# Kernel optimization log

Measured on AMD Instinct MI355X. Metric: run time of the kernel, lower is better.

Reference implementation:

```python
import jax, jax.numpy as jnp
import numpy as np

B, N, FIELD_DIM, OUT_DIM = 65536, 128, 16, 64


def setup_inputs() -> dict:
    key = jax.random.key(0)
    k1, k2 = jax.random.split(key)
    x = jax.random.normal(k1, (B, N), dtype=jnp.float32)
    # learned FFM kernel: (n_features, field_dim, output_dim), uniform init like keras 'uniform'
    kernel = jax.random.uniform(k2, (N, FIELD_DIM, OUT_DIM), dtype=jnp.float32, minval=-0.05, maxval=0.05)
    # feature i belongs to field i % FIELD_DIM (the field_dict of the layer)
    field_dict = jnp.arange(N, dtype=jnp.int32) % FIELD_DIM
    return {"x": x, "kernel": kernel, "field_dict": field_dict}


def reference(x, kernel, field_dict):
    # Original math: out_b = sum_{i<j} <kernel[i, fd[j]], kernel[j, fd[i]]> * x[b,i] * x[b,j]
    n = kernel.shape[0]
    # A[i, j, k] = kernel[i, field_dict[j], k]  -> [N, N, OUT_DIM] (small: 128*128*64)
    A = kernel[:, field_dict, :]
    # S[i, j] = <kernel[i, fd[j]], kernel[j, fd[i]]>
    S = jnp.einsum('ijk,jik->ij', A, A)
    mask = jnp.triu(jnp.ones((n, n), dtype=S.dtype), k=1)  # i < j only
    Sm = S * mask
    # bilinear form per sample: sum_{i<j} S_ij x_i x_j
    return jnp.einsum('bi,ij,bj->b', x, Sm, x)
```

## Files before the change

kernel.cpp:

```cpp
#include <hip/hip_runtime.h>

#define NB 65536
#define NN 128
#define FDIM 16
#define ODIM 64

typedef __attribute__((ext_vector_type(8))) short s16x8;
typedef __attribute__((ext_vector_type(4))) float f32x4;
typedef __attribute__((address_space(3))) void lds_void_t;
typedef const __attribute__((address_space(1))) void gbl_void_t;

__device__ __forceinline__ unsigned short f2bf_rne(float f) {
    unsigned u = __builtin_bit_cast(unsigned, f);
    u += 0x7FFFu + ((u >> 16) & 1u);
    return (unsigned short)(u >> 16);
}
__device__ __forceinline__ float bf2f(unsigned short h) {
    unsigned u = ((unsigned)h) << 16;
    return __builtin_bit_cast(float, u);
}

__device__ __forceinline__ int xswz(int m, int c) {
    int g = (c >> 3) ^ ((m >> 2) << 1);
    return m * 128 + g * 8 + (c & 7);
}

__global__ __launch_bounds__(256) void prep_w_fast(const float* __restrict__ kern,
                                                   const int* __restrict__ fd,
                                                   unsigned short* __restrict__ wfrag) {
    int d = blockIdx.x * 32 + (threadIdx.x >> 3);
    int i = d >> 7, j = d & 127;
    int part = threadIdx.x & 7;
    int fi = fd[i], fj = fd[j];
    const float4* ap = (const float4*)(kern + (i * FDIM + fj) * ODIM + part * 8);
    const float4* bp = (const float4*)(kern + (j * FDIM + fi) * ODIM + part * 8);
    float4 a0 = ap[0], a1 = ap[1];
    float4 b0 = bp[0], b1 = bp[1];
    float s = a0.x * b0.x + a0.y * b0.y + a0.z * b0.z + a0.w * b0.w +
              a1.x * b1.x + a1.y * b1.y + a1.z * b1.z + a1.w * b1.w;
    s += __shfl_xor(s, 1, 64);
    s += __shfl_xor(s, 2, 64);
    s += __shfl_xor(s, 4, 64);
    if (part == 0) {
        float w = (i == j) ? 0.f : 0.5f * s;
        int kt = i >> 5, kc = (i >> 3) & 3, e = i & 7;
        wfrag[(((j >> 4) * 4 + kt) * 64 + kc * 16 + (j & 15)) * 8 + e] = f2bf_rne(w);
    }
}

__global__ __launch_bounds__(256, 2) void qform(const float* __restrict__ x,
                                                const unsigned short* __restrict__ wfrag,
                                                float* __restrict__ out) {
    __shared__ __align__(16) unsigned short wlds[16384];
    __shared__ __align__(16) unsigned short xlds[8][2048];

    const int tid = threadIdx.x;
    const int bid = blockIdx.x;

    {
        const char* gsrc = (const char*)wfrag;
        char* ldst = (char*)wlds;
#pragma unroll
        for (int t = 0; t < 8; ++t) {
            int off = t * 4096 + tid * 16;
            __builtin_amdgcn_global_load_lds((gbl_void_t*)(gsrc + off),
                                             (lds_void_t*)(ldst + off), 16, 0, 0);
        }
    }

    const int wave = tid >> 6, lane = tid & 63;
    const int row = lane & 15, kc = lane >> 4;
    const int t0 = wave * 2, t1 = t0 + 1;
    const size_t base = (size_t)bid * 128;
    const float* xp0 = x + (base + (size_t)(t0 * 16 + row)) * NN;
    const float* xp1 = x + (base + (size_t)(t1 * 16 + row)) * NN;

    s16x8 ah0[4], al0[4], ah1[4], al1[4];
#pragma unroll
    for (int kt = 0; kt < 4; ++kt) {
        const float4* p0 = (const float4*)(xp0 + kt * 32 + kc * 8);
        const float4* p1 = (const float4*)(xp1 + kt * 32 + kc * 8);
        float4 v00 = p0[0], v01 = p0[1], v10 = p1[0], v11 = p1[1];
        float vs0[8] = {v00.x, v00.y, v00.z, v00.w, v01.x, v01.y, v01.z, v01.w};
        float vs1[8] = {v10.x, v10.y, v10.z, v10.w, v11.x, v11.y, v11.z, v11.w};
        s16x8 hv0, hv1;
#pragma unroll
        for (int e = 0; e < 8; ++e) {
            unsigned short h0 = f2bf_rne(vs0[e]);
            unsigned short h1 = f2bf_rne(vs1[e]);
            hv0[e] = (short)h0; hv1[e] = (short)h1;
            ah0[kt][e] = (short)h0; ah1[kt][e] = (short)h1;
            float l0f = vs0[e] - bf2f(h0);
            float l1f = vs1[e] - bf2f(h1);
            al0[kt][e] = (short)(unsigned short)(__builtin_bit_cast(unsigned, l0f) >> 16);
            al1[kt][e] = (short)(unsigned short)(__builtin_bit_cast(unsigned, l1f) >> 16);
        }
        *(s16x8*)&xlds[t0][xswz(row, kt * 32 + kc * 8)] = hv0;
        *(s16x8*)&xlds[t1][xswz(row, kt * 32 + kc * 8)] = hv1;
    }
    __syncthreads();

    f32x4 acc0[8], acc1[8];
#pragma unroll
    for (int nt = 0; nt < 8; ++nt) {
        f32x4 c0 = {0.f, 0.f, 0.f, 0.f}, c1 = {0.f, 0.f, 0.f, 0.f};
#pragma unroll
        for (int kt = 0; kt < 4; ++kt) {
            s16x8 bf = *(const s16x8*)&wlds[((nt * 4 + kt) * 64 + lane) * 8];
            c0 = __builtin_amdgcn_mfma_f32_16x16x32_bf16(ah0[kt], bf, c0, 0, 0, 0);
            c0 = __builtin_amdgcn_mfma_f32_16x16x32_bf16(al0[kt], bf, c0, 0, 0, 0);
            c1 = __builtin_amdgcn_mfma_f32_16x16x32_bf16(ah1[kt], bf, c1, 0, 0, 0);
            c1 = __builtin_amdgcn_mfma_f32_16x16x32_bf16(al1[kt], bf, c1, 0, 0, 0);
        }
        acc0[nt] = c0; acc1[nt] = c1;
    }

    const int rg = lane >> 4, cl = lane & 15;
    float q00 = 0, q01 = 0, q02 = 0, q03 = 0;
    float q10 = 0, q11 = 0, q12 = 0, q13 = 0;
#pragma unroll
    for (int nt = 0; nt < 8; ++nt) {
        int c = nt * 16 + cl;
        q00 += acc0[nt][0] * bf2f(xlds[t0][xswz(rg * 4 + 0, c)]);
        q01 += acc0[nt][1] * bf2f(xlds[t0][xswz(rg * 4 + 1, c)]);
        q02 += acc0[nt][2] * bf2f(xlds[t0][xswz(rg * 4 + 2, c)]);
        q03 += acc0[nt][3] * bf2f(xlds[t0][xswz(rg * 4 + 3, c)]);
        q10 += acc1[nt][0] * bf2f(xlds[t1][xswz(rg * 4 + 0, c)]);
        q11 += acc1[nt][1] * bf2f(xlds[t1][xswz(rg * 4 + 1, c)]);
        q12 += acc1[nt][2] * bf2f(xlds[t1][xswz(rg * 4 + 2, c)]);
        q13 += acc1[nt][3] * bf2f(xlds[t1][xswz(rg * 4 + 3, c)]);
    }
#pragma unroll
    for (int m = 1; m <= 8; m <<= 1) {
        q00 += __shfl_xor(q00, m, 64); q01 += __shfl_xor(q01, m, 64);
        q02 += __shfl_xor(q02, m, 64); q03 += __shfl_xor(q03, m, 64);
        q10 += __shfl_xor(q10, m, 64); q11 += __shfl_xor(q11, m, 64);
        q12 += __shfl_xor(q12, m, 64); q13 += __shfl_xor(q13, m, 64);
    }
    if (cl == 0) {
        float* o0 = out + base + t0 * 16 + rg * 4;
        float* o1 = out + base + t1 * 16 + rg * 4;
        o0[0] = q00; o0[1] = q01; o0[2] = q02; o0[3] = q03;
        o1[0] = q10; o1[1] = q11; o1[2] = q12; o1[3] = q13;
    }
}

extern "C" void kernel_launch(void* const* d_in, const int* in_sizes, int n_in,
                              void* d_out, int out_size, void* d_ws, size_t ws_size,
                              hipStream_t stream) {
    const float* x = (const float*)d_in[0];
    const float* kern = (const float*)d_in[1];
    const int* fd = (const int*)d_in[2];
    float* out = (float*)d_out;
    unsigned short* wfrag = (unsigned short*)d_ws;

    prep_w_fast<<<dim3(512), dim3(256), 0, stream>>>(kern, fd, wfrag);
    qform<<<dim3(512), dim3(256), 0, stream>>>(x, wfrag, out);
}
```

Before: 18.71 us.

## Drop bf16 low-part split MFMAs and re-read fp32 x from global for epilogue

Removes the hi/lo bf16 split of x, so each tile needs half as many MFMAs and fewer registers. The x LDS staging buffer is gone. The epilogue now reads fp32 x straight from global/L2 and fuses the dot products into the MFMA loop instead of holding all accumulators. Occupancy hint rises to 4 blocks and the output store is vectorised. The cost is accuracy: x enters the MFMA only as single bf16, while the epilogue multiplier is now full fp32.

```diff
diff --git a/kernel.cpp b/kernel.cpp
--- a/kernel.cpp
+++ b/kernel.cpp
@@ -14,15 +14,6 @@
     unsigned u = __builtin_bit_cast(unsigned, f);
     u += 0x7FFFu + ((u >> 16) & 1u);
     return (unsigned short)(u >> 16);
-}
-__device__ __forceinline__ float bf2f(unsigned short h) {
-    unsigned u = ((unsigned)h) << 16;
-    return __builtin_bit_cast(float, u);
-}
-
-__device__ __forceinline__ int xswz(int m, int c) {
-    int g = (c >> 3) ^ ((m >> 2) << 1);
-    return m * 128 + g * 8 + (c & 7);
 }
 
 __global__ __launch_bounds__(256) void prep_w_fast(const float* __restrict__ kern,
@@ -48,11 +39,10 @@
     }
 }
 
-__global__ __launch_bounds__(256, 2) void qform(const float* __restrict__ x,
+__global__ __launch_bounds__(256, 4) void qform(const float* __restrict__ x,
                                                 const unsigned short* __restrict__ wfrag,
                                                 float* __restrict__ out) {
     __shared__ __align__(16) unsigned short wlds[16384];
-    __shared__ __align__(16) unsigned short xlds[8][2048];
 
     const int tid = threadIdx.x;
     const int bid = blockIdx.x;
@@ -72,35 +62,31 @@
     const int row = lane & 15, kc = lane >> 4;
     const int t0 = wave * 2, t1 = t0 + 1;
     const size_t base = (size_t)bid * 128;
-    const float* xp0 = x + (base + (size_t)(t0 * 16 + row)) * NN;
-    const float* xp1 = x + (base + (size_t)(t1 * 16 + row)) * NN;
+    const float* xp0 = x + (base + (size_t)(t0 * 16 + row)) * NN + kc * 8;
+    const float* xp1 = x + (base + (size_t)(t1 * 16 + row)) * NN + kc * 8;
 
-    s16x8 ah0[4], al0[4], ah1[4], al1[4];
+    s16x8 ah0[4], ah1[4];
 #pragma unroll
     for (int kt = 0; kt < 4; ++kt) {
-        const float4* p0 = (const float4*)(xp0 + kt * 32 + kc * 8);
-        const float4* p1 = (const float4*)(xp1 + kt * 32 + kc * 8);
+        const float4* p0 = (const float4*)(xp0 + kt * 32);
+        const float4* p1 = (const float4*)(xp1 + kt * 32);
         float4 v00 = p0[0], v01 = p0[1], v10 = p1[0], v11 = p1[1];
         float vs0[8] = {v00.x, v00.y, v00.z, v00.w, v01.x, v01.y, v01.z, v01.w};
         float vs1[8] = {v10.x, v10.y, v10.z, v10.w, v11.x, v11.y, v11.z, v11.w};
-        s16x8 hv0, hv1;
 #pragma unroll
         for (int e = 0; e < 8; ++e) {
-            unsigned short h0 = f2bf_rne(vs0[e]);
-            unsigned short h1 = f2bf_rne(vs1[e]);
-            hv0[e] = (short)h0; hv1[e] = (short)h1;
-            ah0[kt][e] = (short)h0; ah1[kt][e] = (short)h1;
-            float l0f = vs0[e] - bf2f(h0);
-            float l1f = vs1[e] - bf2f(h1);
-            al0[kt][e] = (short)(unsigned short)(__builtin_bit_cast(unsigned, l0f) >> 16);
-            al1[kt][e] = (short)(unsigned short)(__builtin_bit_cast(unsigned, l1f) >> 16);
+            ah0[kt][e] = (short)f2bf_rne(vs0[e]);
+            ah1[kt][e] = (short)f2bf_rne(vs1[e]);
         }
-        *(s16x8*)&xlds[t0][xswz(row, kt * 32 + kc * 8)] = hv0;
-        *(s16x8*)&xlds[t1][xswz(row, kt * 32 + kc * 8)] = hv1;
     }
     __syncthreads();
 
-    f32x4 acc0[8], acc1[8];
+    const int rg = lane >> 4, cl = lane & 15;
+    const float* e0 = x + (base + (size_t)(t0 * 16 + rg * 4)) * NN + cl;
+    const float* e1 = x + (base + (size_t)(t1 * 16 + rg * 4)) * NN + cl;
+
+    float q00 = 0, q01 = 0, q02 = 0, q03 = 0;
+    float q10 = 0, q11 = 0, q12 = 0, q13 = 0;
 #pragma unroll
     for (int nt = 0; nt < 8; ++nt) {
         f32x4 c0 = {0.f, 0.f, 0.f, 0.f}, c1 = {0.f, 0.f, 0.f, 0.f};
@@ -108,27 +94,17 @@
         for (int kt = 0; kt < 4; ++kt) {
             s16x8 bf = *(const s16x8*)&wlds[((nt * 4 + kt) * 64 + lane) * 8];
             c0 = __builtin_amdgcn_mfma_f32_16x16x32_bf16(ah0[kt], bf, c0, 0, 0, 0);
-            c0 = __builtin_amdgcn_mfma_f32_16x16x32_bf16(al0[kt], bf, c0, 0, 0, 0);
             c1 = __builtin_amdgcn_mfma_f32_16x16x32_bf16(ah1[kt], bf, c1, 0, 0, 0);
-            c1 = __builtin_amdgcn_mfma_f32_16x16x32_bf16(al1[kt], bf, c1, 0, 0, 0);
         }
-        acc0[nt] = c0; acc1[nt] = c1;
-    }
-
-    const int rg = lane >> 4, cl = lane & 15;
-    float q00 = 0, q01 = 0, q02 = 0, q03 = 0;
-    float q10 = 0, q11 = 0, q12 = 0, q13 = 0;
-#pragma unroll
-    for (int nt = 0; nt < 8; ++nt) {
-        int c = nt * 16 + cl;
-        q00 += acc0[nt][0] * bf2f(xlds[t0][xswz(rg * 4 + 0, c)]);
-        q01 += acc0[nt][1] * bf2f(xlds[t0][xswz(rg * 4 + 1, c)]);
-        q02 += acc0[nt][2] * bf2f(xlds[t0][xswz(rg * 4 + 2, c)]);
-        q03 += acc0[nt][3] * bf2f(xlds[t0][xswz(rg * 4 + 3, c)]);
-        q10 += acc1[nt][0] * bf2f(xlds[t1][xswz(rg * 4 + 0, c)]);
-        q11 += acc1[nt][1] * bf2f(xlds[t1][xswz(rg * 4 + 1, c)]);
-        q12 += acc1[nt][2] * bf2f(xlds[t1][xswz(rg * 4 + 2, c)]);
-        q13 += acc1[nt][3] * bf2f(xlds[t1][xswz(rg * 4 + 3, c)]);
+        const int nc = nt * 16;
+        q00 += c0[0] * e0[0 * NN + nc];
+        q01 += c0[1] * e0[1 * NN + nc];
+        q02 += c0[2] * e0[2 * NN + nc];
+        q03 += c0[3] * e0[3 * NN + nc];
+        q10 += c1[0] * e1[0 * NN + nc];
+        q11 += c1[1] * e1[1 * NN + nc];
+        q12 += c1[2] * e1[2 * NN + nc];
+        q13 += c1[3] * e1[3 * NN + nc];
     }
 #pragma unroll
     for (int m = 1; m <= 8; m <<= 1) {
@@ -138,10 +114,10 @@
         q12 += __shfl_xor(q12, m, 64); q13 += __shfl_xor(q13, m, 64);
     }
     if (cl == 0) {
-        float* o0 = out + base + t0 * 16 + rg * 4;
-        float* o1 = out + base + t1 * 16 + rg * 4;
-        o0[0] = q00; o0[1] = q01; o0[2] = q02; o0[3] = q03;
-        o1[0] = q10; o1[1] = q11; o1[2] = q12; o1[3] = q13;
+        float4 o0 = {q00, q01, q02, q03};
+        float4 o1 = {q10, q11, q12, q13};
+        *(float4*)(out + base + t0 * 16 + rg * 4) = o0;
+        *(float4*)(out + base + t1 * 16 + rg * 4) = o1;
     }
 }
 
```

Result: faster. 18.05 us, median of 2 (-3.6%).
